# Performance work log

Hardware: AMD Instinct MI355X
Metric: run time of the kernel (lower is better)

The kernel has to match this reference:

```python
import jax, jax.numpy as jnp
import numpy as np

KLD_BINS = 10
RATIO_KLD = 0.5
# categorical one-hot blocks in the 99-dim Adult encoding
BLOCKS = [(1, 8), (8, 24), (24, 31), (31, 45), (45, 51), (51, 53), (53, 55), (58, 99)]
CONT_COLS = np.array([0, 55, 56, 57])


def _cross_entropy(logits, onehot):
    # F.cross_entropy with targets = argmax of the one-hot block (mean over batch)
    logp = jax.nn.log_softmax(logits, axis=-1)
    return -jnp.mean(jnp.sum(onehot * logp, axis=-1))


def _kl_divergence(p, q):
    # np-style KL: sum p*log(p/q) over valid (nonzero) bins
    valid = (p > 0) & (q > 0)
    ratio = jnp.where(valid, p / jnp.where(valid, q, 1.0), 1.0)
    return jnp.sum(jnp.where(valid, p * jnp.log(ratio), 0.0))


def setup_inputs() -> dict:
    B = 262144
    key = jax.random.key(0)
    ks = jax.random.split(key, 16)
    data_decoded = jax.random.normal(ks[0], (B, 99), dtype=jnp.float32)
    # data_true: continuous columns + one-hot categorical blocks
    data_true = jnp.zeros((B, 99), dtype=jnp.float32)
    data_true = data_true.at[:, CONT_COLS].set(jax.random.normal(ks[1], (B, 4), dtype=jnp.float32))
    for j, (s, e) in enumerate(BLOCKS):
        lab = jax.random.randint(ks[2 + j], (B,), 0, e - s)
        data_true = data_true.at[:, s:e].set(jax.nn.one_hot(lab, e - s, dtype=jnp.float32))
    data_encoded = jax.random.normal(ks[11], (B, 12), dtype=jnp.float32)
    sex = jax.random.bernoulli(ks[12], 0.5, (B,)).astype(jnp.float32)
    data_encoded = data_encoded.at[:, 11].set(sex)  # column 11 of combined is the 0/1 sex neuron
    label_true = jax.random.normal(ks[13], (B, 2), dtype=jnp.float32)
    return {
        'data_encoded': data_encoded,
        'data_decoded': data_decoded,
        'data_true': data_true,
        'label_true': label_true,
        'batch_size': B,
    }


def reference(data_encoded, data_decoded, data_true, label_true, batch_size):
    # --- reconstruction MSE on continuous columns ---
    cc = jnp.asarray(CONT_COLS)
    mse_loss = jnp.sum(jnp.mean((data_decoded[:, cc] - data_true[:, cc]) ** 2, axis=0))
    # --- cross-entropy on each categorical block ---
    ce_loss = jnp.float32(0.0)
    for s, e in BLOCKS:
        ce_loss = ce_loss + _cross_entropy(data_decoded[:, s:e], data_true[:, s:e])
    # --- per-feature histogram KLD between male/female groups (no grad, as in torch via .numpy()) ---
    comb = jnp.concatenate([data_encoded, label_true], axis=1)  # [B, 14]
    feats = comb[:, :KLD_BINS]  # first 10 encoded features, [B, 10]
    mn = jnp.min(feats, axis=0)  # per-column min over full batch (torch .item())
    mx = jnp.max(feats, axis=0)
    width = jnp.maximum(mx - mn, 1e-12)
    # torch.histc bin index: floor((x-min)/(max-min)*bins), x==max -> last bin
    idx = jnp.clip(jnp.floor((feats - mn) / width * KLD_BINS).astype(jnp.int32), 0, KLD_BINS - 1)
    onehot = jax.nn.one_hot(idx, KLD_BINS, dtype=jnp.float32)  # [B, 10, bins]
    sexcol = comb[:, 11]
    m_mask = (sexcol == 0).astype(jnp.float32)
    f_mask = (sexcol == 1).astype(jnp.float32)
    m_count = jnp.maximum(jnp.sum(m_mask), 1.0)
    f_count = jnp.maximum(jnp.sum(f_mask), 1.0)
    m_hist = jnp.einsum('b,bik->ik', m_mask, onehot) / m_count  # [10, bins]
    f_hist = jnp.einsum('b,bik->ik', f_mask, onehot) / f_count
    kld = jax.lax.stop_gradient(_kl_divergence(m_hist, f_hist))
    alpha = RATIO_KLD
    multi_loss = (1.0 - alpha) * (mse_loss + ce_loss) + alpha * kld
    return (multi_loss, mse_loss, ce_loss, alpha * kld)
```

## Files before the change

kernel.cpp:

```cpp
#include <hip/hip_runtime.h>
#include <math.h>

#define B_ROWS 262144

#define WS_A 0
#define WS_B 2816
#define WS_C 28416
#define MAIN_BLOCKS 1536
#define N_WAVES (MAIN_BLOCKS * 4)
#define TILE_ROWS 8
#define N_TILES 32768
#define TILE_F4 198

__device__ __forceinline__ unsigned int map_f(float x) {
  unsigned int b = __float_as_uint(x);
  return (b & 0x80000000u) ? ~b : (b | 0x80000000u);
}
__device__ __forceinline__ float unmap_f(unsigned int u) {
  unsigned int b = (u & 0x80000000u) ? (u ^ 0x80000000u) : ~u;
  return __uint_as_float(b);
}

__global__ __launch_bounds__(256) void k_minmax(const float* __restrict__ enc,
                                                unsigned int* __restrict__ ws) {
  int tid = threadIdx.x, bid = blockIdx.x;
  const float4* e4 = (const float4*)enc;
  float mn[10], mx[10];
  #pragma unroll
  for (int j = 0; j < 10; j++) { mn[j] = 1e30f; mx[j] = -1e30f; }
  unsigned int cm = 0, cf = 0;
  #pragma unroll
  for (int i = 0; i < 8; i++) {
    size_t g = (size_t)bid * 2048 + i * 256 + tid;
    float4 a = e4[g * 3 + 0], b = e4[g * 3 + 1], c = e4[g * 3 + 2];
    float v[12] = {a.x,a.y,a.z,a.w,b.x,b.y,b.z,b.w,c.x,c.y,c.z,c.w};
    #pragma unroll
    for (int j = 0; j < 10; j++) { mn[j] = fminf(mn[j], v[j]); mx[j] = fmaxf(mx[j], v[j]); }
    cm += (v[11] == 0.0f); cf += (v[11] == 1.0f);
  }
  #pragma unroll
  for (int off = 32; off; off >>= 1) {
    #pragma unroll
    for (int j = 0; j < 10; j++) {
      mn[j] = fminf(mn[j], __shfl_xor(mn[j], off));
      mx[j] = fmaxf(mx[j], __shfl_xor(mx[j], off));
    }
    cm += __shfl_xor(cm, off); cf += __shfl_xor(cf, off);
  }
  __shared__ float smn[4][10], smx[4][10];
  __shared__ unsigned int sc[4][2];
  int wave = tid >> 6, lane = tid & 63;
  if (lane == 0) {
    #pragma unroll
    for (int j = 0; j < 10; j++) { smn[wave][j] = mn[j]; smx[wave][j] = mx[j]; }
    sc[wave][0] = cm; sc[wave][1] = cf;
  }
  __syncthreads();
  unsigned int* out = ws + WS_A + bid * 22;
  if (tid < 10) {
    float m = fminf(fminf(smn[0][tid], smn[1][tid]), fminf(smn[2][tid], smn[3][tid]));
    out[tid] = map_f(m);
  } else if (tid < 20) {
    int j = tid - 10;
    float m = fmaxf(fmaxf(smx[0][j], smx[1][j]), fmaxf(smx[2][j], smx[3][j]));
    out[tid] = map_f(m);
  } else if (tid < 22) {
    int j = tid - 20;
    out[tid] = sc[0][j] + sc[1][j] + sc[2][j] + sc[3][j];
  }
}

__global__ __launch_bounds__(256) void k_hist(const float* __restrict__ enc,
                                              unsigned int* __restrict__ ws) {
  __shared__ float mnv[10], wid[10];
  __shared__ unsigned int h[200];
  int tid = threadIdx.x, bid = blockIdx.x;
  for (int i = tid; i < 200; i += 256) h[i] = 0u;
  if (tid < 10) {
    unsigned int umn = 0xFFFFFFFFu, umx = 0u;
    #pragma unroll 4
    for (int b = 0; b < 128; b++) {
      umn = min(umn, ws[WS_A + b * 22 + tid]);
      umx = max(umx, ws[WS_A + b * 22 + 10 + tid]);
    }
    float mn = unmap_f(umn);
    mnv[tid] = mn;
    wid[tid] = fmaxf(unmap_f(umx) - mn, 1e-12f);
  }
  __syncthreads();
  const float4* e4 = (const float4*)enc;
  #pragma unroll
  for (int i = 0; i < 8; i++) {
    size_t g = (size_t)bid * 2048 + i * 256 + tid;
    float4 a = e4[g * 3 + 0], b = e4[g * 3 + 1], c = e4[g * 3 + 2];
    float v[12] = {a.x,a.y,a.z,a.w,b.x,b.y,b.z,b.w,c.x,c.y,c.z,c.w};
    int base = (v[11] == 0.0f) ? 0 : ((v[11] == 1.0f) ? 100 : -1);
    if (base >= 0) {
      #pragma unroll
      for (int cc = 0; cc < 10; cc++) {
        float t = (v[cc] - mnv[cc]) / wid[cc] * 10.0f;
        int bi = min(max((int)floorf(t), 0), 9);
        atomicAdd(&h[base + cc * 10 + bi], 1u);
      }
    }
  }
  __syncthreads();
  if (tid < 200) ws[WS_B + bid * 200 + tid] = h[tid];
}

__global__ __launch_bounds__(256, 6) void k_main(const float* __restrict__ d,
                                                 const float* __restrict__ t,
                                                 unsigned int* __restrict__ ws) {
  __shared__ float sd[4][800];
  __shared__ float red[12];
  int tid = threadIdx.x, bid = blockIdx.x;
  int wave = tid >> 6, lane = tid & 63;
  float* ldsd = sd[wave];
  const float4* ld4 = (const float4*)ldsd;
  int gw = bid * 4 + wave;

  float mse = 0.f, dot = 0.f, ce = 0.f;

  for (int tile = gw; tile < N_TILES; tile += N_WAVES) {
    const float4* ds = (const float4*)d + (size_t)tile * TILE_F4;
    const float4* ts = (const float4*)t + (size_t)tile * TILE_F4;
    #pragma unroll
    for (int it = 0; it < 3; ++it)
      __builtin_amdgcn_global_load_lds(
          (const __attribute__((address_space(1))) void*)(ds + it * 64 + lane),
          (__attribute__((address_space(3))) void*)(ldsd + it * 256), 16, 0, 0);
    if (lane < 6)
      __builtin_amdgcn_global_load_lds(
          (const __attribute__((address_space(1))) void*)(ds + 192 + lane),
          (__attribute__((address_space(3))) void*)(ldsd + 768), 16, 0, 0);
    float4 tv0 = ts[lane];
    float4 tv1 = ts[64 + lane];
    float4 tv2 = ts[128 + lane];
    float4 tv3 = (lane < 6) ? ts[192 + lane] : make_float4(0.f, 0.f, 0.f, 0.f);
    asm volatile("s_waitcnt vmcnt(0)" ::: "memory");

    float4 tvv[4] = {tv0, tv1, tv2, tv3};
    #pragma unroll
    for (int it = 0; it < 4; ++it) {
      int f = it * 64 + lane;
      if (f < TILE_F4) {
        float4 xd = ld4[f];
        float4 xt = tvv[it];
        int e = f * 4;
        int c = e - (e / 99) * 99;
        float dv[4] = {xd.x, xd.y, xd.z, xd.w};
        float tw[4] = {xt.x, xt.y, xt.z, xt.w};
        #pragma unroll
        for (int k = 0; k < 4; k++) {
          int cc = c + k;
          if (cc >= 99) cc -= 99;
          bool cont = (cc == 0) | ((unsigned)(cc - 55) <= 2u);
          float diff = dv[k] - tw[k];
          if (cont) mse += diff * diff;
          else      dot += tw[k] * dv[k];
        }
      }
    }
    if (lane < 2 * TILE_ROWS) {
      const float* row = ldsd + (lane >> 1) * 99;
      float Z;
      if ((lane & 1) == 0) {
        Z = 0.f;
        #pragma unroll
        for (int c = 1; c < 8; c++) Z += __expf(row[c]);
        ce += __logf(Z);
        Z = 0.f;
        #pragma unroll
        for (int c = 8; c < 24; c++) Z += __expf(row[c]);
        ce += __logf(Z);
        Z = 0.f;
        #pragma unroll
        for (int c = 24; c < 31; c++) Z += __expf(row[c]);
        ce += __logf(Z);
        Z = 0.f;
        #pragma unroll
        for (int c = 31; c < 45; c++) Z += __expf(row[c]);
        ce += __logf(Z);
        Z = 0.f;
        #pragma unroll
        for (int c = 45; c < 51; c++) Z += __expf(row[c]);
        ce += __logf(Z);
      } else {
        Z = 0.f;
        #pragma unroll
        for (int c = 51; c < 53; c++) Z += __expf(row[c]);
        ce += __logf(Z);
        Z = 0.f;
        #pragma unroll
        for (int c = 53; c < 55; c++) Z += __expf(row[c]);
        ce += __logf(Z);
        Z = 0.f;
        #pragma unroll
        for (int c = 58; c < 99; c++) Z += __expf(row[c]);
        ce += __logf(Z);
      }
    }
  }

  #pragma unroll
  for (int off = 32; off; off >>= 1) {
    mse += __shfl_xor(mse, off);
    dot += __shfl_xor(dot, off);
    ce  += __shfl_xor(ce,  off);
  }
  if (lane == 0) { red[wave] = mse; red[4 + wave] = dot; red[8 + wave] = ce; }
  __syncthreads();
  if (tid == 0) {
    float* C = (float*)(ws + WS_C);
    C[bid]                   = red[0] + red[1] + red[2]  + red[3];
    C[MAIN_BLOCKS + bid]     = red[4] + red[5] + red[6]  + red[7];
    C[2 * MAIN_BLOCKS + bid] = red[8] + red[9] + red[10] + red[11];
  }
}

__global__ __launch_bounds__(256) void k_final(const unsigned int* __restrict__ ws,
                                               float* __restrict__ out) {
  __shared__ float h[200];
  __shared__ float part[256];
  __shared__ float red3[12];
  __shared__ float cnts[2];
  int tid = threadIdx.x;
  if (tid < 200) {
    unsigned int s = 0;
    #pragma unroll 4
    for (int b = 0; b < 128; b++) s += ws[WS_B + b * 200 + tid];
    h[tid] = (float)s;
  }
  if (tid == 200 || tid == 201) {
    unsigned int s = 0;
    #pragma unroll 4
    for (int b = 0; b < 128; b++) s += ws[WS_A + b * 22 + 20 + (tid - 200)];
    cnts[tid - 200] = fmaxf((float)s, 1.0f);
  }
  const float* C = (const float*)(ws + WS_C);
  float msum = 0.f, dsum = 0.f, csum = 0.f;
  for (int i = tid; i < MAIN_BLOCKS; i += 256) {
    msum += C[i]; dsum += C[MAIN_BLOCKS + i]; csum += C[2 * MAIN_BLOCKS + i];
  }
  #pragma unroll
  for (int off = 32; off; off >>= 1) {
    msum += __shfl_xor(msum, off);
    dsum += __shfl_xor(dsum, off);
    csum += __shfl_xor(csum, off);
  }
  int wave = tid >> 6, lane = tid & 63;
  if (lane == 0) { red3[wave] = msum; red3[4 + wave] = dsum; red3[8 + wave] = csum; }
  __syncthreads();
  float term = 0.f;
  if (tid < 100) {
    float mc = h[tid], fc = h[100 + tid];
    if (mc > 0.f && fc > 0.f) {
      float p = mc / cnts[0];
      float q = fc / cnts[1];
      term = p * logf(p / q);
    }
  }
  part[tid] = term;
  __syncthreads();
  for (int s = 128; s; s >>= 1) {
    if (tid < s) part[tid] += part[tid + s];
    __syncthreads();
  }
  if (tid == 0) {
    const float invB = 1.0f / (float)B_ROWS;
    float mse = (red3[0] + red3[1] + red3[2] + red3[3]) * invB;
    float dd  = (red3[4] + red3[5] + red3[6] + red3[7]);
    float cc  = (red3[8] + red3[9] + red3[10] + red3[11]);
    float ce  = (cc - dd) * invB;
    float akld = 0.5f * part[0];
    out[0] = 0.5f * (mse + ce) + akld;
    out[1] = mse;
    out[2] = ce;
    out[3] = akld;
  }
}

extern "C" void kernel_launch(void* const* d_in, const int* in_sizes, int n_in,
                              void* d_out, int out_size, void* d_ws, size_t ws_size,
                              hipStream_t stream) {
  const float* enc = (const float*)d_in[0];
  const float* dec = (const float*)d_in[1];
  const float* tru = (const float*)d_in[2];
  unsigned int* ws = (unsigned int*)d_ws;
  float* out = (float*)d_out;

  hipLaunchKernelGGL(k_minmax, dim3(128),         dim3(256), 0, stream, enc, ws);
  hipLaunchKernelGGL(k_hist,   dim3(128),         dim3(256), 0, stream, enc, ws);
  hipLaunchKernelGGL(k_main,   dim3(MAIN_BLOCKS), dim3(256), 0, stream, dec, tru, ws);
  hipLaunchKernelGGL(k_final,  dim3(1),           dim3(256), 0, stream, ws, out);
}
```

Measured before the change: 268.8 us.

## Fuse all stages into one persistent kernel with double-buffered tile loads

Merges the min/max, histogram, main loss and final reduction kernels into a single launch. 128 prep blocks share global min/max through atomics and a spin barrier among themselves, while the remaining blocks run the MSE/CE pass. The main pass now double-buffers tiles in LDS so the next tile's loads overlap the current compute, and it computes exp once per element in the vectorised pass, storing the results back to LDS for the row sums. A last-block-done counter performs the final reduction, and a memset zeroes the atomic workspace. This removes launch gaps and hides load latency, but relies on all 128 prep blocks being co-resident for the spin barrier and adds a memset call.

```diff
diff --git a/kernel.cpp b/kernel.cpp
--- a/kernel.cpp
+++ b/kernel.cpp
@@ -2,15 +2,16 @@
 #include <math.h>
 
 #define B_ROWS 262144
-
-#define WS_A 0
-#define WS_B 2816
-#define WS_C 28416
-#define MAIN_BLOCKS 1536
+#define PREP_BLOCKS 128
+#define MAIN_BLOCKS 1408
+#define TOTAL_BLOCKS (PREP_BLOCKS + MAIN_BLOCKS)
 #define N_WAVES (MAIN_BLOCKS * 4)
-#define TILE_ROWS 8
-#define N_TILES 32768
+#define N_TILES (B_ROWS / 8)
 #define TILE_F4 198
+
+#define WS_HIST 24
+#define WS_C 256
+#define WS_ZERO_CELLS 224
 
 __device__ __forceinline__ unsigned int map_f(float x) {
   unsigned int b = __float_as_uint(x);
@@ -20,259 +21,292 @@
   unsigned int b = (u & 0x80000000u) ? (u ^ 0x80000000u) : ~u;
   return __uint_as_float(b);
 }
-
-__global__ __launch_bounds__(256) void k_minmax(const float* __restrict__ enc,
-                                                unsigned int* __restrict__ ws) {
-  int tid = threadIdx.x, bid = blockIdx.x;
-  const float4* e4 = (const float4*)enc;
-  float mn[10], mx[10];
-  #pragma unroll
-  for (int j = 0; j < 10; j++) { mn[j] = 1e30f; mx[j] = -1e30f; }
-  unsigned int cm = 0, cf = 0;
-  #pragma unroll
-  for (int i = 0; i < 8; i++) {
-    size_t g = (size_t)bid * 2048 + i * 256 + tid;
-    float4 a = e4[g * 3 + 0], b = e4[g * 3 + 1], c = e4[g * 3 + 2];
-    float v[12] = {a.x,a.y,a.z,a.w,b.x,b.y,b.z,b.w,c.x,c.y,c.z,c.w};
-    #pragma unroll
-    for (int j = 0; j < 10; j++) { mn[j] = fminf(mn[j], v[j]); mx[j] = fmaxf(mx[j], v[j]); }
-    cm += (v[11] == 0.0f); cf += (v[11] == 1.0f);
-  }
-  #pragma unroll
-  for (int off = 32; off; off >>= 1) {
-    #pragma unroll
-    for (int j = 0; j < 10; j++) {
-      mn[j] = fminf(mn[j], __shfl_xor(mn[j], off));
-      mx[j] = fmaxf(mx[j], __shfl_xor(mx[j], off));
-    }
-    cm += __shfl_xor(cm, off); cf += __shfl_xor(cf, off);
-  }
+__device__ __forceinline__ unsigned int aload(const unsigned int* p) {
+  return __hip_atomic_load(p, __ATOMIC_RELAXED, __HIP_MEMORY_SCOPE_AGENT);
+}
+__device__ __forceinline__ float aloadf(const float* p) {
+  return __hip_atomic_load(p, __ATOMIC_RELAXED, __HIP_MEMORY_SCOPE_AGENT);
+}
+
+__device__ __forceinline__ void issue_tile(const float* __restrict__ d,
+                                           const float* __restrict__ t,
+                                           int tile, int lane, float* lb,
+                                           float4& r0, float4& r1,
+                                           float4& r2, float4& r3) {
+  const float4* dsp = (const float4*)d + (size_t)tile * TILE_F4;
+  const float4* tsp = (const float4*)t + (size_t)tile * TILE_F4;
+  __builtin_amdgcn_global_load_lds(
+      (const __attribute__((address_space(1))) void*)(dsp + lane),
+      (__attribute__((address_space(3))) void*)(lb), 16, 0, 0);
+  __builtin_amdgcn_global_load_lds(
+      (const __attribute__((address_space(1))) void*)(dsp + 64 + lane),
+      (__attribute__((address_space(3))) void*)(lb + 256), 16, 0, 0);
+  __builtin_amdgcn_global_load_lds(
+      (const __attribute__((address_space(1))) void*)(dsp + 128 + lane),
+      (__attribute__((address_space(3))) void*)(lb + 512), 16, 0, 0);
+  if (lane < 6)
+    __builtin_amdgcn_global_load_lds(
+        (const __attribute__((address_space(1))) void*)(dsp + 192 + lane),
+        (__attribute__((address_space(3))) void*)(lb + 768), 16, 0, 0);
+  r0 = tsp[lane];
+  r1 = tsp[64 + lane];
+  r2 = tsp[128 + lane];
+  r3 = tsp[192 + ((lane < 6) ? lane : 0)];
+}
+
+template <int IT>
+__device__ __forceinline__ void chunk(const float4* ld4, float4* st4, float4 tv,
+                                      int lane, float& mse, float& dot) {
+  int f = IT * 64 + lane;
+  if (IT < 3 || lane < 6) {
+    float4 xd = ld4[f];
+    int e = f * 4;
+    int c = e - (e / 99) * 99;
+    float dv[4] = {xd.x, xd.y, xd.z, xd.w};
+    float tw[4] = {tv.x, tv.y, tv.z, tv.w};
+#pragma unroll
+    for (int k = 0; k < 4; k++) {
+      int cc = c + k;
+      if (cc >= 99) cc -= 99;
+      bool cont = (cc == 0) | ((unsigned)(cc - 55) <= 2u);
+      float diff = dv[k] - tw[k];
+      if (cont) mse += diff * diff;
+      else      dot += tw[k] * dv[k];
+    }
+    float4 ev;
+    ev.x = __expf(xd.x); ev.y = __expf(xd.y);
+    ev.z = __expf(xd.z); ev.w = __expf(xd.w);
+    st4[f] = ev;
+  }
+}
+
+__global__ __launch_bounds__(256, 6) void k_fused(const float* __restrict__ enc,
+                                                  const float* __restrict__ d,
+                                                  const float* __restrict__ t,
+                                                  unsigned int* __restrict__ ws,
+                                                  float* __restrict__ out) {
+  __shared__ float sd[4][2][800];
+  __shared__ float red[16];
+  __shared__ float mnv[10], wid[10];
+  __shared__ unsigned int h[200];
   __shared__ float smn[4][10], smx[4][10];
   __shared__ unsigned int sc[4][2];
-  int wave = tid >> 6, lane = tid & 63;
-  if (lane == 0) {
-    #pragma unroll
-    for (int j = 0; j < 10; j++) { smn[wave][j] = mn[j]; smx[wave][j] = mx[j]; }
-    sc[wave][0] = cm; sc[wave][1] = cf;
-  }
-  __syncthreads();
-  unsigned int* out = ws + WS_A + bid * 22;
-  if (tid < 10) {
-    float m = fminf(fminf(smn[0][tid], smn[1][tid]), fminf(smn[2][tid], smn[3][tid]));
-    out[tid] = map_f(m);
-  } else if (tid < 20) {
-    int j = tid - 10;
-    float m = fmaxf(fmaxf(smx[0][j], smx[1][j]), fmaxf(smx[2][j], smx[3][j]));
-    out[tid] = map_f(m);
-  } else if (tid < 22) {
-    int j = tid - 20;
-    out[tid] = sc[0][j] + sc[1][j] + sc[2][j] + sc[3][j];
-  }
-}
-
-__global__ __launch_bounds__(256) void k_hist(const float* __restrict__ enc,
-                                              unsigned int* __restrict__ ws) {
-  __shared__ float mnv[10], wid[10];
-  __shared__ unsigned int h[200];
-  int tid = threadIdx.x, bid = blockIdx.x;
-  for (int i = tid; i < 200; i += 256) h[i] = 0u;
-  if (tid < 10) {
-    unsigned int umn = 0xFFFFFFFFu, umx = 0u;
-    #pragma unroll 4
-    for (int b = 0; b < 128; b++) {
-      umn = min(umn, ws[WS_A + b * 22 + tid]);
-      umx = max(umx, ws[WS_A + b * 22 + 10 + tid]);
-    }
-    float mn = unmap_f(umn);
-    mnv[tid] = mn;
-    wid[tid] = fmaxf(unmap_f(umx) - mn, 1e-12f);
-  }
-  __syncthreads();
-  const float4* e4 = (const float4*)enc;
-  #pragma unroll
-  for (int i = 0; i < 8; i++) {
-    size_t g = (size_t)bid * 2048 + i * 256 + tid;
-    float4 a = e4[g * 3 + 0], b = e4[g * 3 + 1], c = e4[g * 3 + 2];
-    float v[12] = {a.x,a.y,a.z,a.w,b.x,b.y,b.z,b.w,c.x,c.y,c.z,c.w};
-    int base = (v[11] == 0.0f) ? 0 : ((v[11] == 1.0f) ? 100 : -1);
-    if (base >= 0) {
-      #pragma unroll
-      for (int cc = 0; cc < 10; cc++) {
-        float t = (v[cc] - mnv[cc]) / wid[cc] * 10.0f;
-        int bi = min(max((int)floorf(t), 0), 9);
-        atomicAdd(&h[base + cc * 10 + bi], 1u);
-      }
-    }
-  }
-  __syncthreads();
-  if (tid < 200) ws[WS_B + bid * 200 + tid] = h[tid];
-}
-
-__global__ __launch_bounds__(256, 6) void k_main(const float* __restrict__ d,
-                                                 const float* __restrict__ t,
-                                                 unsigned int* __restrict__ ws) {
-  __shared__ float sd[4][800];
-  __shared__ float red[12];
+  __shared__ int lastflag;
+
   int tid = threadIdx.x, bid = blockIdx.x;
   int wave = tid >> 6, lane = tid & 63;
-  float* ldsd = sd[wave];
-  const float4* ld4 = (const float4*)ldsd;
-  int gw = bid * 4 + wave;
-
-  float mse = 0.f, dot = 0.f, ce = 0.f;
-
-  for (int tile = gw; tile < N_TILES; tile += N_WAVES) {
-    const float4* ds = (const float4*)d + (size_t)tile * TILE_F4;
-    const float4* ts = (const float4*)t + (size_t)tile * TILE_F4;
-    #pragma unroll
-    for (int it = 0; it < 3; ++it)
-      __builtin_amdgcn_global_load_lds(
-          (const __attribute__((address_space(1))) void*)(ds + it * 64 + lane),
-          (__attribute__((address_space(3))) void*)(ldsd + it * 256), 16, 0, 0);
-    if (lane < 6)
-      __builtin_amdgcn_global_load_lds(
-          (const __attribute__((address_space(1))) void*)(ds + 192 + lane),
-          (__attribute__((address_space(3))) void*)(ldsd + 768), 16, 0, 0);
-    float4 tv0 = ts[lane];
-    float4 tv1 = ts[64 + lane];
-    float4 tv2 = ts[128 + lane];
-    float4 tv3 = (lane < 6) ? ts[192 + lane] : make_float4(0.f, 0.f, 0.f, 0.f);
-    asm volatile("s_waitcnt vmcnt(0)" ::: "memory");
-
-    float4 tvv[4] = {tv0, tv1, tv2, tv3};
-    #pragma unroll
-    for (int it = 0; it < 4; ++it) {
-      int f = it * 64 + lane;
-      if (f < TILE_F4) {
-        float4 xd = ld4[f];
-        float4 xt = tvv[it];
-        int e = f * 4;
-        int c = e - (e / 99) * 99;
-        float dv[4] = {xd.x, xd.y, xd.z, xd.w};
-        float tw[4] = {xt.x, xt.y, xt.z, xt.w};
-        #pragma unroll
-        for (int k = 0; k < 4; k++) {
-          int cc = c + k;
-          if (cc >= 99) cc -= 99;
-          bool cont = (cc == 0) | ((unsigned)(cc - 55) <= 2u);
-          float diff = dv[k] - tw[k];
-          if (cont) mse += diff * diff;
-          else      dot += tw[k] * dv[k];
+
+  if (bid < PREP_BLOCKS) {
+    const float4* e4 = (const float4*)enc;
+    float mn[10], mx[10];
+#pragma unroll
+    for (int j = 0; j < 10; j++) { mn[j] = 1e30f; mx[j] = -1e30f; }
+    unsigned int cm = 0, cf = 0;
+#pragma unroll
+    for (int i = 0; i < 8; i++) {
+      size_t g = (size_t)bid * 2048 + i * 256 + tid;
+      float4 a = e4[g * 3 + 0], b = e4[g * 3 + 1], c = e4[g * 3 + 2];
+      float v[12] = {a.x,a.y,a.z,a.w,b.x,b.y,b.z,b.w,c.x,c.y,c.z,c.w};
+#pragma unroll
+      for (int j = 0; j < 10; j++) { mn[j] = fminf(mn[j], v[j]); mx[j] = fmaxf(mx[j], v[j]); }
+      cm += (v[11] == 0.0f); cf += (v[11] == 1.0f);
+    }
+#pragma unroll
+    for (int off = 32; off; off >>= 1) {
+#pragma unroll
+      for (int j = 0; j < 10; j++) {
+        mn[j] = fminf(mn[j], __shfl_xor(mn[j], off));
+        mx[j] = fmaxf(mx[j], __shfl_xor(mx[j], off));
+      }
+      cm += __shfl_xor(cm, off); cf += __shfl_xor(cf, off);
+    }
+    if (lane == 0) {
+#pragma unroll
+      for (int j = 0; j < 10; j++) { smn[wave][j] = mn[j]; smx[wave][j] = mx[j]; }
+      sc[wave][0] = cm; sc[wave][1] = cf;
+    }
+    __syncthreads();
+    if (tid < 10) {
+      float m = fminf(fminf(smn[0][tid], smn[1][tid]), fminf(smn[2][tid], smn[3][tid]));
+      atomicMax(ws + tid, ~map_f(m));
+    } else if (tid < 20) {
+      int j = tid - 10;
+      float m = fmaxf(fmaxf(smx[0][j], smx[1][j]), fmaxf(smx[2][j], smx[3][j]));
+      atomicMax(ws + tid, map_f(m));
+    } else if (tid < 22) {
+      int j = tid - 20;
+      atomicAdd(ws + 20 + j, sc[0][j] + sc[1][j] + sc[2][j] + sc[3][j]);
+    }
+    __syncthreads();
+    if (tid == 0) {
+      __threadfence();
+      __hip_atomic_fetch_add(ws + 22, 1u, __ATOMIC_ACQ_REL, __HIP_MEMORY_SCOPE_AGENT);
+      while (__hip_atomic_load(ws + 22, __ATOMIC_ACQUIRE, __HIP_MEMORY_SCOPE_AGENT) < PREP_BLOCKS)
+        __builtin_amdgcn_s_sleep(2);
+    }
+    __syncthreads();
+    if (tid < 10) {
+      unsigned int nm = aload(ws + tid);
+      unsigned int xm = aload(ws + 10 + tid);
+      float mn_ = unmap_f(~nm);
+      mnv[tid] = mn_;
+      wid[tid] = fmaxf(unmap_f(xm) - mn_, 1e-12f);
+    }
+    for (int i = tid; i < 200; i += 256) h[i] = 0u;
+    __syncthreads();
+#pragma unroll
+    for (int i = 0; i < 8; i++) {
+      size_t g = (size_t)bid * 2048 + i * 256 + tid;
+      float4 a = e4[g * 3 + 0], b = e4[g * 3 + 1], c = e4[g * 3 + 2];
+      float v[12] = {a.x,a.y,a.z,a.w,b.x,b.y,b.z,b.w,c.x,c.y,c.z,c.w};
+      int base = (v[11] == 0.0f) ? 0 : ((v[11] == 1.0f) ? 100 : -1);
+      if (base >= 0) {
+#pragma unroll
+        for (int cc2 = 0; cc2 < 10; cc2++) {
+          float tt = (v[cc2] - mnv[cc2]) / wid[cc2] * 10.0f;
+          int bi = min(max((int)floorf(tt), 0), 9);
+          atomicAdd(&h[base + cc2 * 10 + bi], 1u);
         }
       }
     }
-    if (lane < 2 * TILE_ROWS) {
-      const float* row = ldsd + (lane >> 1) * 99;
-      float Z;
-      if ((lane & 1) == 0) {
-        Z = 0.f;
-        #pragma unroll
-        for (int c = 1; c < 8; c++) Z += __expf(row[c]);
-        ce += __logf(Z);
-        Z = 0.f;
-        #pragma unroll
-        for (int c = 8; c < 24; c++) Z += __expf(row[c]);
-        ce += __logf(Z);
-        Z = 0.f;
-        #pragma unroll
-        for (int c = 24; c < 31; c++) Z += __expf(row[c]);
-        ce += __logf(Z);
-        Z = 0.f;
-        #pragma unroll
-        for (int c = 31; c < 45; c++) Z += __expf(row[c]);
-        ce += __logf(Z);
-        Z = 0.f;
-        #pragma unroll
-        for (int c = 45; c < 51; c++) Z += __expf(row[c]);
-        ce += __logf(Z);
+    __syncthreads();
+    if (tid < 200) atomicAdd(ws + WS_HIST + tid, h[tid]);
+  } else {
+    int gw = (bid - PREP_BLOCKS) * 4 + wave;
+    float mse = 0.f, dot = 0.f, ce = 0.f;
+    float4 tA0, tA1, tA2, tA3, tB0, tB1, tB2, tB3;
+    int p = 0;
+    int tile = gw;
+    issue_tile(d, t, tile, lane, sd[wave][0], tA0, tA1, tA2, tA3);
+    while (true) {
+      float* cb = sd[wave][p];
+      int next = tile + N_WAVES;
+      bool hn = next < N_TILES;
+      if (hn) {
+        issue_tile(d, t, next, lane, sd[wave][p ^ 1], tB0, tB1, tB2, tB3);
+        asm volatile("s_waitcnt vmcnt(8)" ::: "memory");
       } else {
-        Z = 0.f;
-        #pragma unroll
-        for (int c = 51; c < 53; c++) Z += __expf(row[c]);
-        ce += __logf(Z);
-        Z = 0.f;
-        #pragma unroll
-        for (int c = 53; c < 55; c++) Z += __expf(row[c]);
-        ce += __logf(Z);
-        Z = 0.f;
-        #pragma unroll
-        for (int c = 58; c < 99; c++) Z += __expf(row[c]);
-        ce += __logf(Z);
+        asm volatile("s_waitcnt vmcnt(0)" ::: "memory");
       }
-    }
-  }
-
-  #pragma unroll
-  for (int off = 32; off; off >>= 1) {
-    mse += __shfl_xor(mse, off);
-    dot += __shfl_xor(dot, off);
-    ce  += __shfl_xor(ce,  off);
-  }
-  if (lane == 0) { red[wave] = mse; red[4 + wave] = dot; red[8 + wave] = ce; }
+      __builtin_amdgcn_sched_barrier(0);
+      const float4* ld4 = (const float4*)cb;
+      float4* st4 = (float4*)cb;
+      chunk<0>(ld4, st4, tA0, lane, mse, dot);
+      chunk<1>(ld4, st4, tA1, lane, mse, dot);
+      chunk<2>(ld4, st4, tA2, lane, mse, dot);
+      chunk<3>(ld4, st4, tA3, lane, mse, dot);
+      asm volatile("s_waitcnt lgkmcnt(0)" ::: "memory");
+      __builtin_amdgcn_sched_barrier(0);
+      if (lane < 16) {
+        const float* row = cb + (lane >> 1) * 99;
+        float Z;
+        if ((lane & 1) == 0) {
+          Z = 0.f;
+#pragma unroll
+          for (int c = 1; c < 8; c++) Z += row[c];
+          ce += __logf(Z);
+          Z = 0.f;
+#pragma unroll
+          for (int c = 8; c < 24; c++) Z += row[c];
+          ce += __logf(Z);
+          Z = 0.f;
+#pragma unroll
+          for (int c = 24; c < 31; c++) Z += row[c];
+          ce += __logf(Z);
+          Z = 0.f;
+#pragma unroll
+          for (int c = 31; c < 45; c++) Z += row[c];
+          ce += __logf(Z);
+          Z = 0.f;
+#pragma unroll
+          for (int c = 45; c < 51; c++) Z += row[c];
+          ce += __logf(Z);
+        } else {
+          Z = 0.f;
+#pragma unroll
+          for (int c = 51; c < 53; c++) Z += row[c];
+          ce += __logf(Z);
+          Z = 0.f;
+#pragma unroll
+          for (int c = 53; c < 55; c++) Z += row[c];
+          ce += __logf(Z);
+          float Za = 0.f, Zb = 0.f;
+#pragma unroll
+          for (int c = 58; c < 78; c++) Za += row[c];
+#pragma unroll
+          for (int c = 78; c < 99; c++) Zb += row[c];
+          ce += __logf(Za + Zb);
+        }
+      }
+      if (!hn) break;
+      tile = next;
+      p ^= 1;
+      tA0 = tB0; tA1 = tB1; tA2 = tB2; tA3 = tB3;
+    }
+#pragma unroll
+    for (int off = 32; off; off >>= 1) {
+      mse += __shfl_xor(mse, off);
+      dot += __shfl_xor(dot, off);
+      ce  += __shfl_xor(ce,  off);
+    }
+    if (lane == 0) { red[wave] = mse; red[4 + wave] = dot; red[8 + wave] = ce; }
+    __syncthreads();
+    if (tid == 0) {
+      float* C = (float*)(ws + WS_C);
+      int mb = bid - PREP_BLOCKS;
+      C[mb]                   = red[0] + red[1] + red[2]  + red[3];
+      C[MAIN_BLOCKS + mb]     = red[4] + red[5] + red[6]  + red[7];
+      C[2 * MAIN_BLOCKS + mb] = red[8] + red[9] + red[10] + red[11];
+    }
+  }
+
   __syncthreads();
   if (tid == 0) {
-    float* C = (float*)(ws + WS_C);
-    C[bid]                   = red[0] + red[1] + red[2]  + red[3];
-    C[MAIN_BLOCKS + bid]     = red[4] + red[5] + red[6]  + red[7];
-    C[2 * MAIN_BLOCKS + bid] = red[8] + red[9] + red[10] + red[11];
-  }
-}
-
-__global__ __launch_bounds__(256) void k_final(const unsigned int* __restrict__ ws,
-                                               float* __restrict__ out) {
-  __shared__ float h[200];
-  __shared__ float part[256];
-  __shared__ float red3[12];
-  __shared__ float cnts[2];
-  int tid = threadIdx.x;
-  if (tid < 200) {
-    unsigned int s = 0;
-    #pragma unroll 4
-    for (int b = 0; b < 128; b++) s += ws[WS_B + b * 200 + tid];
-    h[tid] = (float)s;
-  }
-  if (tid == 200 || tid == 201) {
-    unsigned int s = 0;
-    #pragma unroll 4
-    for (int b = 0; b < 128; b++) s += ws[WS_A + b * 22 + 20 + (tid - 200)];
-    cnts[tid - 200] = fmaxf((float)s, 1.0f);
-  }
+    __threadfence();
+    unsigned int old = __hip_atomic_fetch_add(ws + 23, 1u, __ATOMIC_ACQ_REL,
+                                              __HIP_MEMORY_SCOPE_AGENT);
+    lastflag = (old == (unsigned int)(TOTAL_BLOCKS - 1)) ? 1 : 0;
+  }
+  __syncthreads();
+  if (lastflag == 0) return;
+  __threadfence();
+
   const float* C = (const float*)(ws + WS_C);
   float msum = 0.f, dsum = 0.f, csum = 0.f;
   for (int i = tid; i < MAIN_BLOCKS; i += 256) {
-    msum += C[i]; dsum += C[MAIN_BLOCKS + i]; csum += C[2 * MAIN_BLOCKS + i];
-  }
-  #pragma unroll
+    msum += aloadf(C + i);
+    dsum += aloadf(C + MAIN_BLOCKS + i);
+    csum += aloadf(C + 2 * MAIN_BLOCKS + i);
+  }
+  float term = 0.f;
+  if (tid < 100) {
+    float cmf = fmaxf((float)aload(ws + 20), 1.0f);
+    float cff = fmaxf((float)aload(ws + 21), 1.0f);
+    float mc = (float)aload(ws + WS_HIST + tid);
+    float fc = (float)aload(ws + WS_HIST + 100 + tid);
+    if (mc > 0.f && fc > 0.f) {
+      float pp = mc / cmf, qq = fc / cff;
+      term = pp * logf(pp / qq);
+    }
+  }
+#pragma unroll
   for (int off = 32; off; off >>= 1) {
     msum += __shfl_xor(msum, off);
     dsum += __shfl_xor(dsum, off);
     csum += __shfl_xor(csum, off);
-  }
-  int wave = tid >> 6, lane = tid & 63;
-  if (lane == 0) { red3[wave] = msum; red3[4 + wave] = dsum; red3[8 + wave] = csum; }
+    term += __shfl_xor(term, off);
+  }
+  if (lane == 0) {
+    red[wave] = msum; red[4 + wave] = dsum; red[8 + wave] = csum; red[12 + wave] = term;
+  }
   __syncthreads();
-  float term = 0.f;
-  if (tid < 100) {
-    float mc = h[tid], fc = h[100 + tid];
-    if (mc > 0.f && fc > 0.f) {
-      float p = mc / cnts[0];
-      float q = fc / cnts[1];
-      term = p * logf(p / q);
-    }
-  }
-  part[tid] = term;
-  __syncthreads();
-  for (int s = 128; s; s >>= 1) {
-    if (tid < s) part[tid] += part[tid + s];
-    __syncthreads();
-  }
   if (tid == 0) {
     const float invB = 1.0f / (float)B_ROWS;
-    float mse = (red3[0] + red3[1] + red3[2] + red3[3]) * invB;
-    float dd  = (red3[4] + red3[5] + red3[6] + red3[7]);
-    float cc  = (red3[8] + red3[9] + red3[10] + red3[11]);
+    float mse = (red[0] + red[1] + red[2] + red[3]) * invB;
+    float dd  = red[4] + red[5] + red[6] + red[7];
+    float cc  = red[8] + red[9] + red[10] + red[11];
     float ce  = (cc - dd) * invB;
-    float akld = 0.5f * part[0];
+    float akld = 0.5f * (red[12] + red[13] + red[14] + red[15]);
     out[0] = 0.5f * (mse + ce) + akld;
     out[1] = mse;
     out[2] = ce;
@@ -289,8 +323,7 @@
   unsigned int* ws = (unsigned int*)d_ws;
   float* out = (float*)d_out;
 
-  hipLaunchKernelGGL(k_minmax, dim3(128),         dim3(256), 0, stream, enc, ws);
-  hipLaunchKernelGGL(k_hist,   dim3(128),         dim3(256), 0, stream, enc, ws);
-  hipLaunchKernelGGL(k_main,   dim3(MAIN_BLOCKS), dim3(256), 0, stream, dec, tru, ws);
-  hipLaunchKernelGGL(k_final,  dim3(1),           dim3(256), 0, stream, ws, out);
-}
+  hipMemsetAsync(d_ws, 0, WS_ZERO_CELLS * sizeof(unsigned int), stream);
+  hipLaunchKernelGGL(k_fused, dim3(TOTAL_BLOCKS), dim3(256), 0, stream,
+                     enc, dec, tru, ws, out);
+}
```

New measurement: 419.7 us. +56.1%, slower.

## Double-buffer per-wave tile loads into LDS to overlap loads with compute

Applied to the files above, without the earlier changes.

Restructures the main loss loop so each wave prefetches the next tile of both decoded and true data into a second LDS buffer while it computes on the current one. A partial vmcnt wait replaces the full drain. The true-data tile now also goes through direct global-to-LDS loads instead of registers. To fit the larger LDS footprint, the block count is halved and the occupancy hint drops from 6 to 3 blocks per CU, so the total number of tiles in flight stays roughly the same.

```diff
diff --git a/kernel.cpp b/kernel.cpp
--- a/kernel.cpp
+++ b/kernel.cpp
@@ -6,8 +6,8 @@
 #define WS_A 0
 #define WS_B 2816
 #define WS_C 28416
-#define MAIN_BLOCKS 1536
-#define N_WAVES (MAIN_BLOCKS * 4)
+#define MAIN_BLOCKS 768
+#define N_STREAMS (MAIN_BLOCKS * 4)
 #define TILE_ROWS 8
 #define N_TILES 32768
 #define TILE_F4 198
@@ -108,98 +108,129 @@
   if (tid < 200) ws[WS_B + bid * 200 + tid] = h[tid];
 }
 
-__global__ __launch_bounds__(256, 6) void k_main(const float* __restrict__ d,
+__device__ __forceinline__ void issue_tile(const float* __restrict__ d,
+                                           const float* __restrict__ t,
+                                           int tile, int lane,
+                                           float* bd, float* bt) {
+  const float4* dsp = (const float4*)d + (size_t)tile * TILE_F4;
+  const float4* tsp = (const float4*)t + (size_t)tile * TILE_F4;
+  #pragma unroll
+  for (int it = 0; it < 3; ++it) {
+    __builtin_amdgcn_global_load_lds(
+        (const __attribute__((address_space(1))) void*)(dsp + it * 64 + lane),
+        (__attribute__((address_space(3))) void*)(bd + it * 256), 16, 0, 0);
+    __builtin_amdgcn_global_load_lds(
+        (const __attribute__((address_space(1))) void*)(tsp + it * 64 + lane),
+        (__attribute__((address_space(3))) void*)(bt + it * 256), 16, 0, 0);
+  }
+  if (lane < 6) {
+    __builtin_amdgcn_global_load_lds(
+        (const __attribute__((address_space(1))) void*)(dsp + 192 + lane),
+        (__attribute__((address_space(3))) void*)(bd + 768), 16, 0, 0);
+    __builtin_amdgcn_global_load_lds(
+        (const __attribute__((address_space(1))) void*)(tsp + 192 + lane),
+        (__attribute__((address_space(3))) void*)(bt + 768), 16, 0, 0);
+  }
+}
+
+__device__ __forceinline__ void compute_tile(const float* bd, const float* bt,
+                                             int lane,
+                                             float& mse, float& dot, float& ce) {
+  const float4* ld4 = (const float4*)bd;
+  const float4* lt4 = (const float4*)bt;
+  #pragma unroll
+  for (int it = 0; it < 4; ++it) {
+    int f = it * 64 + lane;
+    if (f < TILE_F4) {
+      float4 xd = ld4[f];
+      float4 xt = lt4[f];
+      int e = f * 4;
+      int c = e - (e / 99) * 99;
+      float dv[4] = {xd.x, xd.y, xd.z, xd.w};
+      float tw[4] = {xt.x, xt.y, xt.z, xt.w};
+      #pragma unroll
+      for (int k = 0; k < 4; k++) {
+        int cc = c + k;
+        if (cc >= 99) cc -= 99;
+        bool cont = (cc == 0) | ((unsigned)(cc - 55) <= 2u);
+        float diff = dv[k] - tw[k];
+        if (cont) mse += diff * diff;
+        else      dot += tw[k] * dv[k];
+      }
+    }
+  }
+  if (lane < 2 * TILE_ROWS) {
+    const float* row = bd + (lane >> 1) * 99;
+    float Z;
+    if ((lane & 1) == 0) {
+      Z = 0.f;
+      #pragma unroll
+      for (int c = 1; c < 8; c++) Z += __expf(row[c]);
+      ce += __logf(Z);
+      Z = 0.f;
+      #pragma unroll
+      for (int c = 8; c < 24; c++) Z += __expf(row[c]);
+      ce += __logf(Z);
+      Z = 0.f;
+      #pragma unroll
+      for (int c = 24; c < 31; c++) Z += __expf(row[c]);
+      ce += __logf(Z);
+      Z = 0.f;
+      #pragma unroll
+      for (int c = 31; c < 45; c++) Z += __expf(row[c]);
+      ce += __logf(Z);
+      Z = 0.f;
+      #pragma unroll
+      for (int c = 45; c < 51; c++) Z += __expf(row[c]);
+      ce += __logf(Z);
+    } else {
+      Z = 0.f;
+      #pragma unroll
+      for (int c = 51; c < 53; c++) Z += __expf(row[c]);
+      ce += __logf(Z);
+      Z = 0.f;
+      #pragma unroll
+      for (int c = 53; c < 55; c++) Z += __expf(row[c]);
+      ce += __logf(Z);
+      Z = 0.f;
+      #pragma unroll
+      for (int c = 58; c < 99; c++) Z += __expf(row[c]);
+      ce += __logf(Z);
+    }
+  }
+}
+
+__global__ __launch_bounds__(256, 3) void k_main(const float* __restrict__ d,
                                                  const float* __restrict__ t,
                                                  unsigned int* __restrict__ ws) {
-  __shared__ float sd[4][800];
+  __shared__ float sd[4][2][2][800];
   __shared__ float red[12];
   int tid = threadIdx.x, bid = blockIdx.x;
   int wave = tid >> 6, lane = tid & 63;
-  float* ldsd = sd[wave];
-  const float4* ld4 = (const float4*)ldsd;
+  float* base = &sd[wave][0][0][0];
+
+  float mse = 0.f, dot = 0.f, ce = 0.f;
   int gw = bid * 4 + wave;
 
-  float mse = 0.f, dot = 0.f, ce = 0.f;
-
-  for (int tile = gw; tile < N_TILES; tile += N_WAVES) {
-    const float4* ds = (const float4*)d + (size_t)tile * TILE_F4;
-    const float4* ts = (const float4*)t + (size_t)tile * TILE_F4;
-    #pragma unroll
-    for (int it = 0; it < 3; ++it)
-      __builtin_amdgcn_global_load_lds(
-          (const __attribute__((address_space(1))) void*)(ds + it * 64 + lane),
-          (__attribute__((address_space(3))) void*)(ldsd + it * 256), 16, 0, 0);
-    if (lane < 6)
-      __builtin_amdgcn_global_load_lds(
-          (const __attribute__((address_space(1))) void*)(ds + 192 + lane),
-          (__attribute__((address_space(3))) void*)(ldsd + 768), 16, 0, 0);
-    float4 tv0 = ts[lane];
-    float4 tv1 = ts[64 + lane];
-    float4 tv2 = ts[128 + lane];
-    float4 tv3 = (lane < 6) ? ts[192 + lane] : make_float4(0.f, 0.f, 0.f, 0.f);
-    asm volatile("s_waitcnt vmcnt(0)" ::: "memory");
-
-    float4 tvv[4] = {tv0, tv1, tv2, tv3};
-    #pragma unroll
-    for (int it = 0; it < 4; ++it) {
-      int f = it * 64 + lane;
-      if (f < TILE_F4) {
-        float4 xd = ld4[f];
-        float4 xt = tvv[it];
-        int e = f * 4;
-        int c = e - (e / 99) * 99;
-        float dv[4] = {xd.x, xd.y, xd.z, xd.w};
-        float tw[4] = {xt.x, xt.y, xt.z, xt.w};
-        #pragma unroll
-        for (int k = 0; k < 4; k++) {
-          int cc = c + k;
-          if (cc >= 99) cc -= 99;
-          bool cont = (cc == 0) | ((unsigned)(cc - 55) <= 2u);
-          float diff = dv[k] - tw[k];
-          if (cont) mse += diff * diff;
-          else      dot += tw[k] * dv[k];
-        }
-      }
-    }
-    if (lane < 2 * TILE_ROWS) {
-      const float* row = ldsd + (lane >> 1) * 99;
-      float Z;
-      if ((lane & 1) == 0) {
-        Z = 0.f;
-        #pragma unroll
-        for (int c = 1; c < 8; c++) Z += __expf(row[c]);
-        ce += __logf(Z);
-        Z = 0.f;
-        #pragma unroll
-        for (int c = 8; c < 24; c++) Z += __expf(row[c]);
-        ce += __logf(Z);
-        Z = 0.f;
-        #pragma unroll
-        for (int c = 24; c < 31; c++) Z += __expf(row[c]);
-        ce += __logf(Z);
-        Z = 0.f;
-        #pragma unroll
-        for (int c = 31; c < 45; c++) Z += __expf(row[c]);
-        ce += __logf(Z);
-        Z = 0.f;
-        #pragma unroll
-        for (int c = 45; c < 51; c++) Z += __expf(row[c]);
-        ce += __logf(Z);
-      } else {
-        Z = 0.f;
-        #pragma unroll
-        for (int c = 51; c < 53; c++) Z += __expf(row[c]);
-        ce += __logf(Z);
-        Z = 0.f;
-        #pragma unroll
-        for (int c = 53; c < 55; c++) Z += __expf(row[c]);
-        ce += __logf(Z);
-        Z = 0.f;
-        #pragma unroll
-        for (int c = 58; c < 99; c++) Z += __expf(row[c]);
-        ce += __logf(Z);
-      }
-    }
+  int p = 0;
+  int tile = gw;
+  issue_tile(d, t, tile, lane, base, base + 800);
+  while (tile + N_STREAMS < N_TILES) {
+    int nx = tile + N_STREAMS;
+    float* nb = base + (p ^ 1) * 1600;
+    issue_tile(d, t, nx, lane, nb, nb + 800);
+    asm volatile("s_waitcnt vmcnt(8)" ::: "memory");
+    __builtin_amdgcn_sched_barrier(0);
+    float* cb = base + p * 1600;
+    compute_tile(cb, cb + 800, lane, mse, dot, ce);
+    p ^= 1;
+    tile = nx;
+  }
+  asm volatile("s_waitcnt vmcnt(0)" ::: "memory");
+  __builtin_amdgcn_sched_barrier(0);
+  {
+    float* cb = base + p * 1600;
+    compute_tile(cb, cb + 800, lane, mse, dot, ce);
   }
 
   #pragma unroll
```

Result: slower. 290.3 us (+8.0%).

## Load decoded tile into registers and store per-element exp to LDS for CE

Applied to the files above, without the earlier changes.

Drops the asynchronous global-to-LDS load and reads the decoded tile straight into registers. Every lane now computes exp of its four elements and writes them to the wave's LDS buffer, so the 16 cross-entropy lanes only sum stored exponentials and take logs. This spreads the transcendental work across all 64 lanes instead of 16, and splits the long final block sum into two partial chains. The cost is exp on continuous columns that are never used, extra LDS writes, and a same-wave LDS write-then-read that relies on wave-level ordering without an explicit barrier.

```diff
diff --git a/kernel.cpp b/kernel.cpp
--- a/kernel.cpp
+++ b/kernel.cpp
@@ -116,7 +116,7 @@
   int tid = threadIdx.x, bid = blockIdx.x;
   int wave = tid >> 6, lane = tid & 63;
   float* ldsd = sd[wave];
-  const float4* ld4 = (const float4*)ldsd;
+  float4* lw4 = (float4*)ldsd;
   int gw = bid * 4 + wave;
 
   float mse = 0.f, dot = 0.f, ce = 0.f;
@@ -124,28 +124,19 @@
   for (int tile = gw; tile < N_TILES; tile += N_WAVES) {
     const float4* ds = (const float4*)d + (size_t)tile * TILE_F4;
     const float4* ts = (const float4*)t + (size_t)tile * TILE_F4;
-    #pragma unroll
-    for (int it = 0; it < 3; ++it)
-      __builtin_amdgcn_global_load_lds(
-          (const __attribute__((address_space(1))) void*)(ds + it * 64 + lane),
-          (__attribute__((address_space(3))) void*)(ldsd + it * 256), 16, 0, 0);
-    if (lane < 6)
-      __builtin_amdgcn_global_load_lds(
-          (const __attribute__((address_space(1))) void*)(ds + 192 + lane),
-          (__attribute__((address_space(3))) void*)(ldsd + 768), 16, 0, 0);
-    float4 tv0 = ts[lane];
-    float4 tv1 = ts[64 + lane];
-    float4 tv2 = ts[128 + lane];
-    float4 tv3 = (lane < 6) ? ts[192 + lane] : make_float4(0.f, 0.f, 0.f, 0.f);
-    asm volatile("s_waitcnt vmcnt(0)" ::: "memory");
-
-    float4 tvv[4] = {tv0, tv1, tv2, tv3};
+    int cl = (lane < 6) ? lane : 0;
+    float4 d0 = ds[lane],       t0 = ts[lane];
+    float4 d1 = ds[64 + lane],  t1 = ts[64 + lane];
+    float4 d2 = ds[128 + lane], t2 = ts[128 + lane];
+    float4 d3 = ds[192 + cl],   t3 = ts[192 + cl];
+    float4 dv4[4] = {d0, d1, d2, d3};
+    float4 tv4[4] = {t0, t1, t2, t3};
     #pragma unroll
     for (int it = 0; it < 4; ++it) {
-      int f = it * 64 + lane;
-      if (f < TILE_F4) {
-        float4 xd = ld4[f];
-        float4 xt = tvv[it];
+      if (it < 3 || lane < 6) {
+        int f = it * 64 + lane;
+        float4 xd = dv4[it];
+        float4 xt = tv4[it];
         int e = f * 4;
         int c = e - (e / 99) * 99;
         float dv[4] = {xd.x, xd.y, xd.z, xd.w};
@@ -159,6 +150,10 @@
           if (cont) mse += diff * diff;
           else      dot += tw[k] * dv[k];
         }
+        float4 ev;
+        ev.x = __expf(xd.x); ev.y = __expf(xd.y);
+        ev.z = __expf(xd.z); ev.w = __expf(xd.w);
+        lw4[f] = ev;
       }
     }
     if (lane < 2 * TILE_ROWS) {
@@ -167,37 +162,39 @@
       if ((lane & 1) == 0) {
         Z = 0.f;
         #pragma unroll
-        for (int c = 1; c < 8; c++) Z += __expf(row[c]);
-        ce += __logf(Z);
-        Z = 0.f;
-        #pragma unroll
-        for (int c = 8; c < 24; c++) Z += __expf(row[c]);
-        ce += __logf(Z);
-        Z = 0.f;
-        #pragma unroll
-        for (int c = 24; c < 31; c++) Z += __expf(row[c]);
-        ce += __logf(Z);
-        Z = 0.f;
-        #pragma unroll
-        for (int c = 31; c < 45; c++) Z += __expf(row[c]);
-        ce += __logf(Z);
-        Z = 0.f;
-        #pragma unroll
-        for (int c = 45; c < 51; c++) Z += __expf(row[c]);
+        for (int c = 1; c < 8; c++) Z += row[c];
+        ce += __logf(Z);
+        Z = 0.f;
+        #pragma unroll
+        for (int c = 8; c < 24; c++) Z += row[c];
+        ce += __logf(Z);
+        Z = 0.f;
+        #pragma unroll
+        for (int c = 24; c < 31; c++) Z += row[c];
+        ce += __logf(Z);
+        Z = 0.f;
+        #pragma unroll
+        for (int c = 31; c < 45; c++) Z += row[c];
+        ce += __logf(Z);
+        Z = 0.f;
+        #pragma unroll
+        for (int c = 45; c < 51; c++) Z += row[c];
         ce += __logf(Z);
       } else {
         Z = 0.f;
         #pragma unroll
-        for (int c = 51; c < 53; c++) Z += __expf(row[c]);
-        ce += __logf(Z);
-        Z = 0.f;
-        #pragma unroll
-        for (int c = 53; c < 55; c++) Z += __expf(row[c]);
-        ce += __logf(Z);
-        Z = 0.f;
-        #pragma unroll
-        for (int c = 58; c < 99; c++) Z += __expf(row[c]);
-        ce += __logf(Z);
+        for (int c = 51; c < 53; c++) Z += row[c];
+        ce += __logf(Z);
+        Z = 0.f;
+        #pragma unroll
+        for (int c = 53; c < 55; c++) Z += row[c];
+        ce += __logf(Z);
+        float Za = 0.f, Zb = 0.f;
+        #pragma unroll
+        for (int c = 58; c < 78; c++) Za += row[c];
+        #pragma unroll
+        for (int c = 78; c < 99; c++) Zb += row[c];
+        ce += __logf(Za + Zb);
       }
     }
   }
```

Result: no change. 266.8 us (-0.8%).
